# Kernel tuning notes

Measured on AMD Instinct MI355X. Metric: run time of the kernel, lower is better.

The kernel has to match this reference:

```python
import jax, jax.numpy as jnp
import numpy as np
import math

D_MODEL = 1024
N_HEADS = 16
D_HEAD = D_MODEL // N_HEADS
D_FF = 4 * D_MODEL
EPS = 1e-5


def layer_norm(x, gamma, beta):
    mu = jnp.mean(x, axis=-1, keepdims=True)
    var = jnp.var(x, axis=-1, keepdims=True)
    return (x - mu) * jax.lax.rsqrt(var + EPS) * gamma + beta


def setup_inputs() -> dict:
    key = jax.random.key(0)
    ks = jax.random.split(key, 8)
    B, C, D = 32, 256, D_MODEL
    s = 0.02
    return {
        "X": jax.random.normal(ks[0], (B, C, D), dtype=jnp.float32),
        "W_qkv": jax.random.normal(ks[1], (D, 3 * D), dtype=jnp.float32) * s,
        "b_qkv": jnp.zeros((3 * D,), dtype=jnp.float32),
        "W_proj": jax.random.normal(ks[2], (D, D), dtype=jnp.float32) * s,
        "b_proj": jnp.zeros((D,), dtype=jnp.float32),
        "g1": jnp.ones((D,), dtype=jnp.float32),
        "beta1": jnp.zeros((D,), dtype=jnp.float32),
        "g2": jnp.ones((D,), dtype=jnp.float32),
        "beta2": jnp.zeros((D,), dtype=jnp.float32),
        "W_ff1": jax.random.normal(ks[3], (D, D_FF), dtype=jnp.float32) * s,
        "b_ff1": jnp.zeros((D_FF,), dtype=jnp.float32),
        "W_ff2": jax.random.normal(ks[4], (D_FF, D), dtype=jnp.float32) * s,
        "b_ff2": jnp.zeros((D,), dtype=jnp.float32),
    }


def reference(X, W_qkv, b_qkv, W_proj, b_proj, g1, beta1, g2, beta2,
              W_ff1, b_ff1, W_ff2, b_ff2):
    B, C, D = X.shape
    H, Dh = N_HEADS, D_HEAD
    scale = 1.0 / math.sqrt(Dh)

    Xn = layer_norm(X, g1, beta1)
    qkv = Xn @ W_qkv + b_qkv                       # [B, C, 3D]
    q, k, v = jnp.split(qkv, 3, axis=-1)
    # split heads -> [B, H, C, Dh]
    sh = lambda t: t.reshape(B, C, H, Dh).transpose(0, 2, 1, 3)
    q, k, v = sh(q), sh(k), sh(v)

    scores = jnp.einsum("bhcd,bhkd->bhck", q, k) * scale  # [B, H, C, C]
    attn = jax.nn.softmax(scores, axis=-1)
    ctx = jnp.einsum("bhck,bhkd->bhcd", attn, v)           # [B, H, C, Dh]
    ctx = ctx.transpose(0, 2, 1, 3).reshape(B, C, D)

    X1 = X + (ctx @ W_proj + b_proj)
    X2n = layer_norm(X1, g2, beta2)
    h = jax.nn.gelu(X2n @ W_ff1 + b_ff1, approximate=False)
    X_out = X1 + (h @ W_ff2 + b_ff2)
    A = attn.mean(axis=1)                                   # [B, C, C]
    return (X_out, A)
```

## Files before the change

### kernel.cpp

```cpp
#include <hip/hip_runtime.h>
#include <cstdint>
#include <cstddef>

typedef short bf16x8 __attribute__((ext_vector_type(8)));
typedef float f32x4 __attribute__((ext_vector_type(4)));
typedef unsigned short u16;
typedef u16 u16x8 __attribute__((ext_vector_type(8)));
typedef u16 u16x4 __attribute__((ext_vector_type(4)));

#define GLD16(gptr, lptr)                                                            \
  __builtin_amdgcn_global_load_lds((const __attribute__((address_space(1))) void*)(gptr), \
                                   (__attribute__((address_space(3))) void*)(lptr), 16, 0, 0)

__device__ __forceinline__ u16 f2bf(float f) {
  union { float f; unsigned u; } v; v.f = f;
  unsigned r = v.u + 0x7FFF + ((v.u >> 16) & 1);
  return (u16)(r >> 16);
}
__device__ __forceinline__ float bf2f(u16 h) {
  union { unsigned u; float f; } v; v.u = ((unsigned)h) << 16;
  return v.f;
}

__device__ __forceinline__ f32x4 mfma16(bf16x8 a, bf16x8 b, f32x4 c) {
  return __builtin_amdgcn_mfma_f32_16x16x32_bf16(a, b, c, 0, 0, 0);
}

__device__ __forceinline__ bf16x8 lds_read_sw64(const u16* base, int row, int col) {
  int byt = row * 128 + col * 2;
  byt ^= (row & 7) << 4;
  return *(const bf16x8*)((const char*)base + byt);
}

__global__ __launch_bounds__(256) void transpose_cast(const float* __restrict__ in,
                                                      u16* __restrict__ out, int R, int C) {
  __shared__ float tile[32][33];
  const int tx = threadIdx.x, ty = threadIdx.y;
  const int c0 = blockIdx.x * 32, r0 = blockIdx.y * 32;
#pragma unroll
  for (int i = 0; i < 32; i += 8)
    tile[ty + i][tx] = in[(size_t)(r0 + ty + i) * C + c0 + tx];
  __syncthreads();
#pragma unroll
  for (int i = 0; i < 32; i += 8)
    out[(size_t)(c0 + ty + i) * R + r0 + tx] = f2bf(tile[tx][ty + i]);
}

__global__ __launch_bounds__(256) void layernorm_bf16(const float* __restrict__ X,
                                                      const float* __restrict__ g,
                                                      const float* __restrict__ be,
                                                      u16* __restrict__ out) {
  const int row = blockIdx.x, t = threadIdx.x;
  const int lane = t & 63, wave = t >> 6;
  const float* x = X + (size_t)row * 1024;
  __shared__ float part[4];
  float v[4]; float s = 0.f;
#pragma unroll
  for (int i = 0; i < 4; ++i) { v[i] = x[t + i * 256]; s += v[i]; }
#pragma unroll
  for (int o = 32; o >= 1; o >>= 1) s += __shfl_xor(s, o);
  if (lane == 0) part[wave] = s;
  __syncthreads();
  const float mu = (part[0] + part[1] + part[2] + part[3]) * (1.f / 1024.f);
  float d2 = 0.f;
#pragma unroll
  for (int i = 0; i < 4; ++i) { float d = v[i] - mu; d2 += d * d; }
#pragma unroll
  for (int o = 32; o >= 1; o >>= 1) d2 += __shfl_xor(d2, o);
  __syncthreads();
  if (lane == 0) part[wave] = d2;
  __syncthreads();
  const float var = (part[0] + part[1] + part[2] + part[3]) * (1.f / 1024.f);
  const float rstd = rsqrtf(var + 1e-5f);
#pragma unroll
  for (int i = 0; i < 4; ++i) {
    const int c = t + i * 256;
    out[(size_t)row * 1024 + c] = f2bf((v[i] - mu) * rstd * g[c] + be[c]);
  }
}

__global__ __launch_bounds__(256) void layernorm_bb(const u16* __restrict__ Xb,
                                                    const float* __restrict__ g,
                                                    const float* __restrict__ be,
                                                    u16* __restrict__ out) {
  const int row = blockIdx.x, t = threadIdx.x;
  const int lane = t & 63, wave = t >> 6;
  __shared__ float part[4];
  const u16x4 xv = *(const u16x4*)(Xb + (size_t)row * 1024 + t * 4);
  float v[4]; float s = 0.f;
#pragma unroll
  for (int i = 0; i < 4; ++i) { v[i] = bf2f(xv[i]); s += v[i]; }
#pragma unroll
  for (int o = 32; o >= 1; o >>= 1) s += __shfl_xor(s, o);
  if (lane == 0) part[wave] = s;
  __syncthreads();
  const float mu = (part[0] + part[1] + part[2] + part[3]) * (1.f / 1024.f);
  float d2 = 0.f;
#pragma unroll
  for (int i = 0; i < 4; ++i) { float d = v[i] - mu; d2 += d * d; }
#pragma unroll
  for (int o = 32; o >= 1; o >>= 1) d2 += __shfl_xor(d2, o);
  __syncthreads();
  if (lane == 0) part[wave] = d2;
  __syncthreads();
  const float var = (part[0] + part[1] + part[2] + part[3]) * (1.f / 1024.f);
  const float rstd = rsqrtf(var + 1e-5f);
#pragma unroll
  for (int i = 0; i < 4; ++i) {
    const int c = t * 4 + i;
    out[(size_t)row * 1024 + c] = f2bf((v[i] - mu) * rstd * g[c] + be[c]);
  }
}

template <int EPI>
__global__ __launch_bounds__(256, 2) void gemm_sb(const u16* __restrict__ A,
                                                  const u16* __restrict__ Bt,
                                                  const float* __restrict__ bias,
                                                  u16* __restrict__ outb,
                                                  int M, int N, int K) {
  constexpr int ABYT = 128 * 128;
  __shared__ __attribute__((aligned(16))) char lds[2 * ABYT];

  const int t = threadIdx.x, lane = t & 63, wave = t >> 6;
  const int wm = wave >> 1, wn = wave & 1;
  const int l15 = lane & 15, l16 = lane >> 4;

  const int xcd = (int)blockIdx.x & 7, q = (int)blockIdx.x >> 3;
  const int j = q & 63, gq = q >> 6;
  const int g = gq * 8 + xcd;
  const int NGN = N >> 10;
  const int gm = g / NGN, gn = g % NGN;
  const int bm = (gm * 8 + (j >> 3)) * 128;
  const int bn = (gn * 8 + (j & 7)) * 128;

  const u16* aptr[4];
  const u16* bptr[4];
#pragma unroll
  for (int c = 0; c < 4; ++c) {
    int Lb = c * 4096 + t * 16;
    int x = (Lb ^ ((Lb >> 3) & 0x70)) >> 1;
    aptr[c] = A + (size_t)(bm + (x >> 6)) * K + (x & 63);
    bptr[c] = Bt + (size_t)(bn + (x >> 6)) * K + (x & 63);
  }

  auto stage = [&](int p) {
    const int ko = p * 64;
    char* ab = lds + t * 16;
    char* bb = lds + ABYT + t * 16;
#pragma unroll
    for (int c = 0; c < 4; ++c) GLD16(aptr[c] + ko, ab + c * 4096);
#pragma unroll
    for (int c = 0; c < 4; ++c) GLD16(bptr[c] + ko, bb + c * 4096);
  };

  const int co0 = l16 * 16, co1 = 64 + l16 * 16;
  f32x4 acc[4][4] = {};
  const int nkt = K >> 6;

#pragma unroll 1
  for (int kt = 0; kt < nkt; ++kt) {
    __syncthreads();
    stage(kt);
    __syncthreads();

    const char* ab = lds;
    const char* bb = lds + ABYT;
#pragma unroll
    for (int ks = 0; ks < 2; ++ks) {
      const int co = ks ? co1 : co0;
      bf16x8 a[4], b[4];
#pragma unroll
      for (int m = 0; m < 4; ++m) {
        const int r = wm * 64 + m * 16 + l15;
        a[m] = *(const bf16x8*)(ab + r * 128 + (co ^ ((r & 7) << 4)));
      }
#pragma unroll
      for (int n = 0; n < 4; ++n) {
        const int r = wn * 64 + n * 16 + l15;
        b[n] = *(const bf16x8*)(bb + r * 128 + (co ^ ((r & 7) << 4)));
      }
#pragma unroll
      for (int m = 0; m < 4; ++m)
#pragma unroll
        for (int n = 0; n < 4; ++n)
          acc[m][n] = mfma16(a[m], b[n], acc[m][n]);
    }
  }

  const int r0 = l16 * 4;
#pragma unroll
  for (int m = 0; m < 4; ++m) {
#pragma unroll
    for (int n = 0; n < 4; ++n) {
      const int col = bn + wn * 64 + n * 16 + l15;
      const float bv = bias[col];
#pragma unroll
      for (int r = 0; r < 4; ++r) {
        const int row = bm + wm * 64 + m * 16 + r0 + r;
        const float v = acc[m][n][r] + bv;
        const size_t o = (size_t)row * N + col;
        if (EPI == 0) {
          outb[o] = f2bf(v);
        } else {
          const float u = 0.7978845608f * (v + 0.044715f * v * v * v);
          const float e = __expf(2.f * u);
          const float th = 1.f - 2.f / (1.f + e);
          outb[o] = f2bf(0.5f * v * (1.f + th));
        }
      }
    }
  }
}

template <int EPI>
__global__ __launch_bounds__(256, 2) void gemm_128(const u16* __restrict__ A,
                                                   const u16* __restrict__ Bt,
                                                   const float* __restrict__ bias,
                                                   const float* __restrict__ resf,
                                                   const u16* __restrict__ resb,
                                                   float* __restrict__ outf,
                                                   u16* __restrict__ outb,
                                                   int M, int N, int K) {
  constexpr int ABYT = 128 * 128;
  __shared__ __attribute__((aligned(16))) char lds[4 * ABYT];

  const int t = threadIdx.x, lane = t & 63, wave = t >> 6;
  const int wm = wave >> 1, wn = wave & 1;
  const int l15 = lane & 15, l16 = lane >> 4;

  const int xcd = (int)blockIdx.x & 7, q = (int)blockIdx.x >> 3;
  const int j = q & 63, gq = q >> 6;
  const int g = gq * 8 + xcd;
  const int NGN = N >> 10;
  const int gm = g / NGN, gn = g % NGN;
  const int bm = (gm * 8 + (j >> 3)) * 128;
  const int bn = (gn * 8 + (j & 7)) * 128;

  const u16* aptr[4];
  const u16* bptr[4];
#pragma unroll
  for (int c = 0; c < 4; ++c) {
    int Lb = c * 4096 + t * 16;
    int x = (Lb ^ ((Lb >> 3) & 0x70)) >> 1;
    aptr[c] = A + (size_t)(bm + (x >> 6)) * K + (x & 63);
    bptr[c] = Bt + (size_t)(bn + (x >> 6)) * K + (x & 63);
  }

  auto stage = [&](int p) {
    const int ko = p * 64;
    const int s = p & 1;
    char* ab = lds + s * ABYT + t * 16;
    char* bb = lds + 2 * ABYT + s * ABYT + t * 16;
#pragma unroll
    for (int c = 0; c < 4; ++c) GLD16(aptr[c] + ko, ab + c * 4096);
#pragma unroll
    for (int c = 0; c < 4; ++c) GLD16(bptr[c] + ko, bb + c * 4096);
  };
  stage(0);

  const int co0 = l16 * 16, co1 = 64 + l16 * 16;
  f32x4 acc[4][4] = {};
  const int nkt = K >> 6;

#pragma unroll 1
  for (int kt = 0; kt < nkt; ++kt) {
    asm volatile("s_waitcnt vmcnt(0)" ::: "memory");
    asm volatile("s_barrier" ::: "memory");
    if (kt + 1 < nkt) stage(kt + 1);

    const int s = kt & 1;
    const char* ab = lds + s * ABYT;
    const char* bb = lds + 2 * ABYT + s * ABYT;
#pragma unroll
    for (int ks = 0; ks < 2; ++ks) {
      const int co = ks ? co1 : co0;
      bf16x8 a[4], b[4];
#pragma unroll
      for (int m = 0; m < 4; ++m) {
        const int r = wm * 64 + m * 16 + l15;
        a[m] = *(const bf16x8*)(ab + r * 128 + (co ^ ((r & 7) << 4)));
      }
#pragma unroll
      for (int n = 0; n < 4; ++n) {
        const int r = wn * 64 + n * 16 + l15;
        b[n] = *(const bf16x8*)(bb + r * 128 + (co ^ ((r & 7) << 4)));
      }
      __builtin_amdgcn_s_setprio(1);
#pragma unroll
      for (int m = 0; m < 4; ++m)
#pragma unroll
        for (int n = 0; n < 4; ++n)
          acc[m][n] = mfma16(a[m], b[n], acc[m][n]);
      __builtin_amdgcn_s_setprio(0);
    }
  }

  const int r0 = l16 * 4;
#pragma unroll
  for (int m = 0; m < 4; ++m) {
#pragma unroll
    for (int n = 0; n < 4; ++n) {
      const int col = bn + wn * 64 + n * 16 + l15;
      const float bv = bias[col];
#pragma unroll
      for (int r = 0; r < 4; ++r) {
        const int row = bm + wm * 64 + m * 16 + r0 + r;
        const float v = acc[m][n][r] + bv;
        const size_t o = (size_t)row * N + col;
        if (EPI == 3) {
          outf[o] = bf2f(resb[o]) + v;
        } else {
          outb[o] = f2bf(resf[o] + v);
        }
      }
    }
  }
}

__global__ __launch_bounds__(256) void attn_scores(const u16* __restrict__ qkv,
                                                   u16* __restrict__ probs) {
  __shared__ u16 Ks[256 * 64];
  __shared__ u16 Qs[64 * 64];
  const int t = threadIdx.x, lane = t & 63, wave = t >> 6;
  const int qb = blockIdx.x * 64, h = blockIdx.y, b = blockIdx.z;
  const size_t row0 = (size_t)b * 256 * 3072;

#pragma unroll
  for (int is = 0; is < 8; ++is) {
    int L = (is * 2048 + t * 8) * 2;
    int x = (L ^ ((L >> 3) & 0x70)) >> 1;
    int kk = x >> 6, d = x & 63;
    const u16* gp = qkv + row0 + (size_t)kk * 3072 + 1024 + h * 64 + d;
    GLD16(gp, (char*)Ks + is * 4096 + wave * 1024);
  }
#pragma unroll
  for (int is = 0; is < 2; ++is) {
    int L = (is * 2048 + t * 8) * 2;
    int x = (L ^ ((L >> 3) & 0x70)) >> 1;
    int q = x >> 6, d = x & 63;
    const u16* gp = qkv + row0 + (size_t)(qb + q) * 3072 + h * 64 + d;
    GLD16(gp, (char*)Qs + is * 4096 + wave * 1024);
  }
  __syncthreads();

  f32x4 acc[16] = {};
  bf16x8 aq[2];
#pragma unroll
  for (int ks = 0; ks < 2; ++ks)
    aq[ks] = lds_read_sw64(Qs, wave * 16 + (lane & 15), ks * 32 + (lane >> 4) * 8);
#pragma unroll
  for (int nf = 0; nf < 16; ++nf) {
#pragma unroll
    for (int ks = 0; ks < 2; ++ks) {
      bf16x8 bk = lds_read_sw64(Ks, nf * 16 + (lane & 15), ks * 32 + (lane >> 4) * 8);
      acc[nf] = mfma16(aq[ks], bk, acc[nf]);
    }
  }

  const int r0 = (lane >> 4) * 4, cc = lane & 15;
  const float sc = 0.125f;
#pragma unroll
  for (int r = 0; r < 4; ++r) {
    float mx = -1e30f;
#pragma unroll
    for (int nf = 0; nf < 16; ++nf) mx = fmaxf(mx, acc[nf][r]);
#pragma unroll
    for (int o = 8; o >= 1; o >>= 1) mx = fmaxf(mx, __shfl_xor(mx, o));
    float s = 0.f;
#pragma unroll
    for (int nf = 0; nf < 16; ++nf) {
      float e = __expf((acc[nf][r] - mx) * sc);
      acc[nf][r] = e; s += e;
    }
#pragma unroll
    for (int o = 8; o >= 1; o >>= 1) s += __shfl_xor(s, o);
    const float rinv = 1.f / s;
    const int qrow = qb + wave * 16 + r0 + r;
    u16* prow = probs + (size_t)((b * 16 + h) * 256 + qrow) * 256;
#pragma unroll
    for (int nf = 0; nf < 16; ++nf)
      prow[nf * 16 + cc] = f2bf(acc[nf][r] * rinv);
  }
}

__global__ __launch_bounds__(256) void amean(const u16* __restrict__ probs,
                                             float* __restrict__ A) {
  const int bq = blockIdx.x;
  const int b = bq >> 8, q = bq & 255;
  const int t = threadIdx.x;
  float s = 0.f;
#pragma unroll
  for (int h = 0; h < 16; ++h)
    s += bf2f(probs[(size_t)((b * 16 + h) * 256 + q) * 256 + t]);
  A[(size_t)bq * 256 + t] = s * (1.f / 16.f);
}

__global__ __launch_bounds__(256) void attn_pv(const u16* __restrict__ qkv,
                                               const u16* __restrict__ probs,
                                               u16* __restrict__ ctx) {
  __shared__ u16 Vs[64 * 256];
  const int t = threadIdx.x, lane = t & 63, wave = t >> 6;
  const int h = blockIdx.x, b = blockIdx.y;

#pragma unroll
  for (int p = 0; p < 8; ++p) {
    int idx = p * 2048 + t * 8;
    int kk = idx >> 6, d0 = idx & 63;
    u16x8 vv = *(const u16x8*)(qkv + (size_t)(b * 256 + kk) * 3072 + 2048 + h * 64 + d0);
#pragma unroll
    for (int j = 0; j < 8; ++j) {
      int d = d0 + j;
      int byt = (d * 512 + kk * 2) ^ ((d & 7) << 4);
      *(u16*)((char*)Vs + byt) = vv[j];
    }
  }
  __syncthreads();

  f32x4 acc[4][4] = {};
  const u16* Pb = probs + (size_t)((b * 16 + h) * 256) * 256;
  const int cc = lane & 15, kg = (lane >> 4) * 8;
#pragma unroll
  for (int kt = 0; kt < 8; ++kt) {
    bf16x8 a[4], v[4];
#pragma unroll
    for (int m = 0; m < 4; ++m)
      a[m] = *(const bf16x8*)(Pb + (size_t)(wave * 64 + m * 16 + cc) * 256 + kt * 32 + kg);
#pragma unroll
    for (int n = 0; n < 4; ++n) {
      int d = n * 16 + cc;
      int kk = kt * 32 + kg;
      int byt = (d * 512 + kk * 2) ^ ((d & 7) << 4);
      v[n] = *(const bf16x8*)((const char*)Vs + byt);
    }
#pragma unroll
    for (int m = 0; m < 4; ++m)
#pragma unroll
      for (int n = 0; n < 4; ++n)
        acc[m][n] = mfma16(a[m], v[n], acc[m][n]);
  }

  const int r0 = (lane >> 4) * 4;
#pragma unroll
  for (int m = 0; m < 4; ++m) {
    const int q = wave * 64 + m * 16 + r0;
#pragma unroll
    for (int n = 0; n < 4; ++n) {
      const int col = h * 64 + n * 16 + cc;
#pragma unroll
      for (int r = 0; r < 4; ++r)
        ctx[(size_t)(b * 256 + q + r) * 1024 + col] = f2bf(acc[m][n][r]);
    }
  }
}

extern "C" void kernel_launch(void* const* d_in, const int* in_sizes, int n_in,
                              void* d_out, int out_size, void* d_ws, size_t ws_size,
                              hipStream_t stream) {
  const float* X      = (const float*)d_in[0];
  const float* W_qkv  = (const float*)d_in[1];
  const float* b_qkv  = (const float*)d_in[2];
  const float* W_proj = (const float*)d_in[3];
  const float* b_proj = (const float*)d_in[4];
  const float* g1     = (const float*)d_in[5];
  const float* beta1  = (const float*)d_in[6];
  const float* g2     = (const float*)d_in[7];
  const float* beta2  = (const float*)d_in[8];
  const float* W_ff1  = (const float*)d_in[9];
  const float* b_ff1  = (const float*)d_in[10];
  const float* W_ff2  = (const float*)d_in[11];
  const float* b_ff2  = (const float*)d_in[12];

  float* Xout = (float*)d_out;
  float* Aout = (float*)d_out + 8388608;

  char* ws = (char*)d_ws;
  const size_t MB = 1u << 20;
  u16* xn    = (u16*)(ws + 0);
  u16* wqkv  = (u16*)(ws + 16 * MB);
  u16* wproj = (u16*)(ws + 22 * MB);
  u16* wff1  = (u16*)(ws + 24 * MB);
  u16* wff2  = (u16*)(ws + 32 * MB);
  u16* qkv   = (u16*)(ws + 40 * MB);
  u16* probs = (u16*)(ws + 88 * MB);
  u16* hbuf  = probs;
  u16* x1b   = (u16*)(ws + 152 * MB);
  u16* ctx   = xn;
  u16* x1n   = xn;

  const dim3 tb(32, 8);
  transpose_cast<<<dim3(96, 32),  tb, 0, stream>>>(W_qkv,  wqkv, 1024, 3072);
  transpose_cast<<<dim3(32, 32),  tb, 0, stream>>>(W_proj, wproj, 1024, 1024);
  transpose_cast<<<dim3(128, 32), tb, 0, stream>>>(W_ff1,  wff1, 1024, 4096);
  transpose_cast<<<dim3(32, 128), tb, 0, stream>>>(W_ff2,  wff2, 4096, 1024);

  layernorm_bf16<<<8192, 256, 0, stream>>>(X, g1, beta1, xn);

  gemm_sb<0><<<1536, 256, 0, stream>>>(xn, wqkv, b_qkv, qkv, 8192, 3072, 1024);

  attn_scores<<<dim3(4, 16, 32), 256, 0, stream>>>(qkv, probs);
  amean<<<8192, 256, 0, stream>>>(probs, Aout);
  attn_pv<<<dim3(16, 32), 256, 0, stream>>>(qkv, probs, ctx);

  gemm_128<4><<<512, 256, 0, stream>>>(ctx, wproj, b_proj, X, nullptr, nullptr, x1b,
                                       8192, 1024, 1024);

  layernorm_bb<<<8192, 256, 0, stream>>>(x1b, g2, beta2, x1n);

  gemm_sb<2><<<2048, 256, 0, stream>>>(x1n, wff1, b_ff1, hbuf, 8192, 4096, 1024);

  gemm_128<3><<<512, 256, 0, stream>>>(hbuf, wff2, b_ff2, nullptr, x1b, Xout, nullptr,
                                       8192, 1024, 4096);
}
```

Before: 333.0 us.

## Fuse attention score/softmax and PV kernels into one per-head kernel

Merges attn_scores and attn_pv into a single kernel per (batch, head) that computes scores, softmax, writes probs, stages them in LDS and immediately multiplies by V. This removes the global reread of the probability tensor in the PV stage and one kernel launch. In exchange the grid shrinks to one block per head with 128KB of LDS, limiting occupancy and serializing the four query chunks within a block.

```diff
diff --git a/kernel.cpp b/kernel.cpp
--- a/kernel.cpp
+++ b/kernel.cpp
@@ -317,69 +317,115 @@
   }
 }
 
-__global__ __launch_bounds__(256) void attn_scores(const u16* __restrict__ qkv,
-                                                   u16* __restrict__ probs) {
+__global__ __launch_bounds__(256) void attn_spv(const u16* __restrict__ qkv,
+                                                u16* __restrict__ probs,
+                                                u16* __restrict__ ctx) {
   __shared__ u16 Ks[256 * 64];
-  __shared__ u16 Qs[64 * 64];
+  __shared__ u16 Qs[256 * 64];
+  __shared__ u16 Vs[64 * 256];
+  __shared__ u16 Ps[64 * 256];
   const int t = threadIdx.x, lane = t & 63, wave = t >> 6;
-  const int qb = blockIdx.x * 64, h = blockIdx.y, b = blockIdx.z;
-  const size_t row0 = (size_t)b * 256 * 3072;
+  const int l15 = lane & 15, l16 = lane >> 4;
+  const int h = blockIdx.x, b = blockIdx.y;
+  const size_t base = (size_t)b * 256 * 3072;
 
 #pragma unroll
   for (int is = 0; is < 8; ++is) {
     int L = (is * 2048 + t * 8) * 2;
     int x = (L ^ ((L >> 3) & 0x70)) >> 1;
     int kk = x >> 6, d = x & 63;
-    const u16* gp = qkv + row0 + (size_t)kk * 3072 + 1024 + h * 64 + d;
-    GLD16(gp, (char*)Ks + is * 4096 + wave * 1024);
-  }
-#pragma unroll
-  for (int is = 0; is < 2; ++is) {
-    int L = (is * 2048 + t * 8) * 2;
-    int x = (L ^ ((L >> 3) & 0x70)) >> 1;
-    int q = x >> 6, d = x & 63;
-    const u16* gp = qkv + row0 + (size_t)(qb + q) * 3072 + h * 64 + d;
-    GLD16(gp, (char*)Qs + is * 4096 + wave * 1024);
-  }
-  __syncthreads();
-
-  f32x4 acc[16] = {};
-  bf16x8 aq[2];
-#pragma unroll
-  for (int ks = 0; ks < 2; ++ks)
-    aq[ks] = lds_read_sw64(Qs, wave * 16 + (lane & 15), ks * 32 + (lane >> 4) * 8);
-#pragma unroll
-  for (int nf = 0; nf < 16; ++nf) {
-#pragma unroll
-    for (int ks = 0; ks < 2; ++ks) {
-      bf16x8 bk = lds_read_sw64(Ks, nf * 16 + (lane & 15), ks * 32 + (lane >> 4) * 8);
-      acc[nf] = mfma16(aq[ks], bk, acc[nf]);
-    }
-  }
-
-  const int r0 = (lane >> 4) * 4, cc = lane & 15;
+    GLD16(qkv + base + (size_t)kk * 3072 + 1024 + h * 64 + d,
+          (char*)Ks + is * 4096 + wave * 1024);
+    GLD16(qkv + base + (size_t)kk * 3072 + h * 64 + d,
+          (char*)Qs + is * 4096 + wave * 1024);
+  }
+#pragma unroll
+  for (int p = 0; p < 8; ++p) {
+    const int idx = p * 2048 + t * 8;
+    const int kk = idx >> 6, d0 = idx & 63;
+    const u16x8 vv = *(const u16x8*)(qkv + base + (size_t)kk * 3072 + 2048 + h * 64 + d0);
+#pragma unroll
+    for (int jj = 0; jj < 8; ++jj) {
+      const int d = d0 + jj;
+      const int byt = (d * 512 + kk * 2) ^ ((d & 7) << 4);
+      *(u16*)((char*)Vs + byt) = vv[jj];
+    }
+  }
+  __syncthreads();
+
+  const int r0 = l16 * 4;
   const float sc = 0.125f;
-#pragma unroll
-  for (int r = 0; r < 4; ++r) {
-    float mx = -1e30f;
-#pragma unroll
-    for (int nf = 0; nf < 16; ++nf) mx = fmaxf(mx, acc[nf][r]);
-#pragma unroll
-    for (int o = 8; o >= 1; o >>= 1) mx = fmaxf(mx, __shfl_xor(mx, o));
-    float s = 0.f;
+
+#pragma unroll 1
+  for (int qc = 0; qc < 4; ++qc) {
+    const int qw = qc * 64 + wave * 16;
+
+    f32x4 acc[16] = {};
+    bf16x8 aq[2];
+#pragma unroll
+    for (int ks = 0; ks < 2; ++ks)
+      aq[ks] = lds_read_sw64(Qs, qw + l15, ks * 32 + l16 * 8);
 #pragma unroll
     for (int nf = 0; nf < 16; ++nf) {
-      float e = __expf((acc[nf][r] - mx) * sc);
-      acc[nf][r] = e; s += e;
-    }
-#pragma unroll
-    for (int o = 8; o >= 1; o >>= 1) s += __shfl_xor(s, o);
-    const float rinv = 1.f / s;
-    const int qrow = qb + wave * 16 + r0 + r;
-    u16* prow = probs + (size_t)((b * 16 + h) * 256 + qrow) * 256;
-#pragma unroll
-    for (int nf = 0; nf < 16; ++nf)
-      prow[nf * 16 + cc] = f2bf(acc[nf][r] * rinv);
+#pragma unroll
+      for (int ks = 0; ks < 2; ++ks) {
+        bf16x8 bk = lds_read_sw64(Ks, nf * 16 + l15, ks * 32 + l16 * 8);
+        acc[nf] = mfma16(aq[ks], bk, acc[nf]);
+      }
+    }
+
+#pragma unroll
+    for (int r = 0; r < 4; ++r) {
+      float mx = -1e30f;
+#pragma unroll
+      for (int nf = 0; nf < 16; ++nf) mx = fmaxf(mx, acc[nf][r]);
+#pragma unroll
+      for (int o = 8; o >= 1; o >>= 1) mx = fmaxf(mx, __shfl_xor(mx, o));
+      float s = 0.f;
+#pragma unroll
+      for (int nf = 0; nf < 16; ++nf) {
+        const float e = __expf((acc[nf][r] - mx) * sc);
+        acc[nf][r] = e; s += e;
+      }
+#pragma unroll
+      for (int o = 8; o >= 1; o >>= 1) s += __shfl_xor(s, o);
+      const float rinv = 1.f / s;
+      const int qrow = qc * 64 + wave * 16 + r0 + r;
+      const int lrow = wave * 16 + r0 + r;
+      u16* prow = probs + (size_t)((b * 16 + h) * 256 + qrow) * 256;
+#pragma unroll
+      for (int nf = 0; nf < 16; ++nf) {
+        const u16 pb = f2bf(acc[nf][r] * rinv);
+        prow[nf * 16 + l15] = pb;
+        const int byt = (lrow * 512 + (nf * 16 + l15) * 2) ^ ((lrow & 7) << 4);
+        *(u16*)((char*)Ps + byt) = pb;
+      }
+    }
+
+    f32x4 cacc[4] = {};
+#pragma unroll
+    for (int kt = 0; kt < 8; ++kt) {
+      const int prow = wave * 16 + l15;
+      const int pbyt = (prow * 512 + kt * 64 + l16 * 16) ^ ((prow & 7) << 4);
+      const bf16x8 a = *(const bf16x8*)((const char*)Ps + pbyt);
+#pragma unroll
+      for (int n = 0; n < 4; ++n) {
+        const int d = n * 16 + l15;
+        const int kk = kt * 32 + l16 * 8;
+        const int vbyt = (d * 512 + kk * 2) ^ ((d & 7) << 4);
+        const bf16x8 v = *(const bf16x8*)((const char*)Vs + vbyt);
+        cacc[n] = mfma16(a, v, cacc[n]);
+      }
+    }
+#pragma unroll
+    for (int n = 0; n < 4; ++n) {
+      const int col = h * 64 + n * 16 + l15;
+#pragma unroll
+      for (int r = 0; r < 4; ++r) {
+        const int qrow = qc * 64 + wave * 16 + r0 + r;
+        ctx[(size_t)(b * 256 + qrow) * 1024 + col] = f2bf(cacc[n][r]);
+      }
+    }
   }
 }
 
@@ -393,64 +439,6 @@
   for (int h = 0; h < 16; ++h)
     s += bf2f(probs[(size_t)((b * 16 + h) * 256 + q) * 256 + t]);
   A[(size_t)bq * 256 + t] = s * (1.f / 16.f);
-}
-
-__global__ __launch_bounds__(256) void attn_pv(const u16* __restrict__ qkv,
-                                               const u16* __restrict__ probs,
-                                               u16* __restrict__ ctx) {
-  __shared__ u16 Vs[64 * 256];
-  const int t = threadIdx.x, lane = t & 63, wave = t >> 6;
-  const int h = blockIdx.x, b = blockIdx.y;
-
-#pragma unroll
-  for (int p = 0; p < 8; ++p) {
-    int idx = p * 2048 + t * 8;
-    int kk = idx >> 6, d0 = idx & 63;
-    u16x8 vv = *(const u16x8*)(qkv + (size_t)(b * 256 + kk) * 3072 + 2048 + h * 64 + d0);
-#pragma unroll
-    for (int j = 0; j < 8; ++j) {
-      int d = d0 + j;
-      int byt = (d * 512 + kk * 2) ^ ((d & 7) << 4);
-      *(u16*)((char*)Vs + byt) = vv[j];
-    }
-  }
-  __syncthreads();
-
-  f32x4 acc[4][4] = {};
-  const u16* Pb = probs + (size_t)((b * 16 + h) * 256) * 256;
-  const int cc = lane & 15, kg = (lane >> 4) * 8;
-#pragma unroll
-  for (int kt = 0; kt < 8; ++kt) {
-    bf16x8 a[4], v[4];
-#pragma unroll
-    for (int m = 0; m < 4; ++m)
-      a[m] = *(const bf16x8*)(Pb + (size_t)(wave * 64 + m * 16 + cc) * 256 + kt * 32 + kg);
-#pragma unroll
-    for (int n = 0; n < 4; ++n) {
-      int d = n * 16 + cc;
-      int kk = kt * 32 + kg;
-      int byt = (d * 512 + kk * 2) ^ ((d & 7) << 4);
-      v[n] = *(const bf16x8*)((const char*)Vs + byt);
-    }
-#pragma unroll
-    for (int m = 0; m < 4; ++m)
-#pragma unroll
-      for (int n = 0; n < 4; ++n)
-        acc[m][n] = mfma16(a[m], v[n], acc[m][n]);
-  }
-
-  const int r0 = (lane >> 4) * 4;
-#pragma unroll
-  for (int m = 0; m < 4; ++m) {
-    const int q = wave * 64 + m * 16 + r0;
-#pragma unroll
-    for (int n = 0; n < 4; ++n) {
-      const int col = h * 64 + n * 16 + cc;
-#pragma unroll
-      for (int r = 0; r < 4; ++r)
-        ctx[(size_t)(b * 256 + q + r) * 1024 + col] = f2bf(acc[m][n][r]);
-    }
-  }
 }
 
 extern "C" void kernel_launch(void* const* d_in, const int* in_sizes, int n_in,
@@ -497,9 +485,8 @@
 
   gemm_sb<0><<<1536, 256, 0, stream>>>(xn, wqkv, b_qkv, qkv, 8192, 3072, 1024);
 
-  attn_scores<<<dim3(4, 16, 32), 256, 0, stream>>>(qkv, probs);
+  attn_spv<<<dim3(16, 32), 256, 0, stream>>>(qkv, probs, ctx);
   amean<<<8192, 256, 0, stream>>>(probs, Aout);
-  attn_pv<<<dim3(16, 32), 256, 0, stream>>>(qkv, probs, ctx);
 
   gemm_128<4><<<512, 256, 0, stream>>>(ctx, wproj, b_proj, X, nullptr, nullptr, x1b,
                                        8192, 1024, 1024);
```

After: 338.8 us. Within noise of the previous version (+1.7%).
